# Kernel optimization log

Hardware: AMD Instinct MI355X
Metric: run time of the kernel (lower is better)

The kernel has to match this reference:

```python
import jax, jax.numpy as jnp
import numpy as np

N, C, DFF, TMAX = 4, 768, 3072, 20
RMS_EPS = 1e-6
SINK_EPS = 1e-6
POST_MULT = 2.0


def setup_inputs() -> dict:
    key = jax.random.key(0)
    ks = jax.random.split(key, 5)
    B, S = 4, 4096
    x = jax.random.normal(ks[0], (B, S, N, C), dtype=jnp.float32)
    phi = jax.random.normal(ks[1], (N * C, N * N + 2 * N), dtype=jnp.float32) * 0.02
    b = jnp.zeros((N * N + 2 * N,), dtype=jnp.float32)
    alpha_pre = jnp.ones((1,), dtype=jnp.float32)
    alpha_post = jnp.ones((1,), dtype=jnp.float32)
    alpha_res = jnp.ones((1,), dtype=jnp.float32)
    W1 = jax.random.normal(ks[2], (C, DFF), dtype=jnp.float32) * (1.0 / np.sqrt(C))
    b1 = jnp.zeros((DFF,), dtype=jnp.float32)
    W2 = jax.random.normal(ks[3], (DFF, C), dtype=jnp.float32) * (1.0 / np.sqrt(DFF))
    b2 = jnp.zeros((C,), dtype=jnp.float32)
    return {"x": x, "phi": phi, "b": b, "alpha_pre": alpha_pre,
            "alpha_post": alpha_post, "alpha_res": alpha_res,
            "W1": W1, "b1": b1, "W2": W2, "b2": b2}


def _sinkhorn(logits):
    # logits: (..., 16) -> doubly-stochastic (..., 4, 4); rows = logits[..., 4i:4i+4]
    r = logits.reshape(*logits.shape[:-1], N, N)
    r = jnp.exp(r - jnp.max(r, axis=-1, keepdims=True))
    for _ in range(TMAX):
        r = r / (jnp.sum(r, axis=-1, keepdims=True) + SINK_EPS)  # row normalize
        r = r / (jnp.sum(r, axis=-2, keepdims=True) + SINK_EPS)  # column normalize
    return r


def _mhc_forward(x, phi, b, alpha_pre, alpha_post, alpha_res, W1, b1, W2, b2):
    lead = x.shape[:-2]
    x_mat = x.reshape(-1, N * C)
    # fused RMS-norm + linear routing projection
    invr = jax.lax.rsqrt(jnp.mean(x_mat * x_mat, axis=-1, keepdims=True) + RMS_EPS)
    mix = (x_mat @ phi) * invr  # (T, n^2 + 2n)
    h_pre = jax.nn.sigmoid(mix[:, :N] * alpha_pre + b[:N]).reshape(*lead, N)
    h_post = (jax.nn.sigmoid(mix[:, N:2 * N] * alpha_post + b[N:2 * N]) * POST_MULT).reshape(*lead, N)
    h_res = _sinkhorn(mix[:, 2 * N:] * alpha_res + b[2 * N:]).reshape(*lead, N, N)
    # pre-aggregate n streams -> single full-width stream
    x_in = jnp.einsum('...nc,...n->...c', x, h_pre)
    # wrapped sublayer: baseline MLP at full width
    f_out = jax.nn.gelu(x_in @ W1 + b1, approximate=False) @ W2 + b2
    # residual stream mixing + post scatter
    res_gather = jnp.einsum('...ij,...jc->...ic', h_res, x)
    return res_gather + h_post[..., None] * f_out[..., None, :]


def reference(x, phi, b, alpha_pre, alpha_post, alpha_res, W1, b1, W2, b2):
    return _mhc_forward(x, phi, b, alpha_pre, alpha_post, alpha_res, W1, b1, W2, b2)
```

## Files before the change

### kernel.cpp

```cpp
#include <hip/hip_runtime.h>
#include <hip/hip_bf16.h>
#include <stdint.h>

#define NT   16384
#define C_   768
#define DFF_ 3072
#define KX   3072
#define NMIX 24

typedef __attribute__((ext_vector_type(8))) short shortx8;
typedef __attribute__((ext_vector_type(4))) float floatx4;

__device__ __forceinline__ short f2bf(float f) {
  union { float f; uint32_t u; } v; v.f = f;
  uint32_t r = v.u + 0x7fffu + ((v.u >> 16) & 1u);
  return (short)(r >> 16);
}

__global__ void phiT_kernel(const float* __restrict__ phi, float* __restrict__ phiT) {
  int idx = blockIdx.x * 256 + threadIdx.x;
  if (idx < KX * NMIX) {
    int k = idx / NMIX, j = idx - k * NMIX;
    phiT[(size_t)j * KX + k] = phi[idx];
  }
}

__global__ __launch_bounds__(256) void transpose_bf16(const float* __restrict__ in,
                                                      short* __restrict__ out,
                                                      int R, int C) {
  __shared__ float tile[32][33];
  int bx = blockIdx.x * 32;
  int by = blockIdx.y * 32;
  int tx = threadIdx.x & 31, ty = threadIdx.x >> 5;
  #pragma unroll
  for (int i = 0; i < 32; i += 8)
    tile[ty + i][tx] = in[(size_t)(by + ty + i) * C + bx + tx];
  __syncthreads();
  #pragma unroll
  for (int i = 0; i < 32; i += 8)
    out[(size_t)(bx + ty + i) * R + by + tx] = f2bf(tile[tx][ty + i]);
}

#define TB 64
__global__ __launch_bounds__(256) void k1(
    const float* __restrict__ x, const float* __restrict__ phiT,
    const float* __restrict__ bvec, const float* __restrict__ a_pre,
    const float* __restrict__ a_post, const float* __restrict__ a_res,
    short* __restrict__ x_in, float* __restrict__ hpost, float* __restrict__ hres) {
  __shared__ float xs[TB][132];
  __shared__ float invr_s[TB];
  __shared__ float mixs[TB][NMIX];
  __shared__ float hpre_s[TB][4];
  int tid = threadIdx.x;
  int lane = tid & 63;
  int w = tid >> 6;
  int wu = __builtin_amdgcn_readfirstlane(w);
  int t0 = blockIdx.x * TB;

  float acc[6] = {0.f, 0.f, 0.f, 0.f, 0.f, 0.f};
  float ssq = 0.f;

  for (int kc = 0; kc < KX; kc += 128) {
    if (kc) __syncthreads();
    #pragma unroll
    for (int jj = 0; jj < 8; ++jj) {
      int idx = tid + jj * 256;
      int row = idx >> 5, c4 = idx & 31;
      const float4 v = *(const float4*)&x[(size_t)(t0 + row) * KX + kc + c4 * 4];
      *(float4*)&xs[row][c4 * 4] = v;
    }
    __syncthreads();
    #pragma unroll 4
    for (int k4 = 0; k4 < 32; ++k4) {
      const float4 xv = *(const float4*)&xs[lane][k4 * 4];
      if (w == 0) ssq += xv.x * xv.x + xv.y * xv.y + xv.z * xv.z + xv.w * xv.w;
      int kk = kc + k4 * 4;
      #pragma unroll
      for (int jj = 0; jj < 6; ++jj) {
        const float4 p = *(const float4*)&phiT[(size_t)(wu * 6 + jj) * KX + kk];
        acc[jj] += p.x * xv.x + p.y * xv.y + p.z * xv.z + p.w * xv.w;
      }
    }
  }
  if (w == 0) invr_s[lane] = rsqrtf(ssq * (1.0f / KX) + 1e-6f);
  #pragma unroll
  for (int jj = 0; jj < 6; ++jj) mixs[lane][w * 6 + jj] = acc[jj];
  __syncthreads();

  {
    int tq = tid >> 2, r = tid & 3;
    float invr = invr_s[tq];
    float ares = a_res[0];
    float v0 = mixs[tq][8 + r * 4 + 0] * invr * ares + bvec[8 + r * 4 + 0];
    float v1 = mixs[tq][8 + r * 4 + 1] * invr * ares + bvec[8 + r * 4 + 1];
    float v2 = mixs[tq][8 + r * 4 + 2] * invr * ares + bvec[8 + r * 4 + 2];
    float v3 = mixs[tq][8 + r * 4 + 3] * invr * ares + bvec[8 + r * 4 + 3];
    float mx = fmaxf(fmaxf(v0, v1), fmaxf(v2, v3));
    v0 = __expf(v0 - mx); v1 = __expf(v1 - mx); v2 = __expf(v2 - mx); v3 = __expf(v3 - mx);
    for (int it = 0; it < 20; ++it) {
      float s = v0 + v1 + v2 + v3 + 1e-6f;
      float inv = 1.0f / s;
      v0 *= inv; v1 *= inv; v2 *= inv; v3 *= inv;
      float c0 = v0 + __shfl_xor(v0, 1); c0 += __shfl_xor(c0, 2);
      float c1 = v1 + __shfl_xor(v1, 1); c1 += __shfl_xor(c1, 2);
      float c2 = v2 + __shfl_xor(v2, 1); c2 += __shfl_xor(c2, 2);
      float c3 = v3 + __shfl_xor(v3, 1); c3 += __shfl_xor(c3, 2);
      v0 /= (c0 + 1e-6f); v1 /= (c1 + 1e-6f); v2 /= (c2 + 1e-6f); v3 /= (c3 + 1e-6f);
    }
    float* ho = hres + (size_t)(t0 + tq) * 16 + r * 4;
    ho[0] = v0; ho[1] = v1; ho[2] = v2; ho[3] = v3;
    if (r == 0) {
      float apre = a_pre[0];
      #pragma unroll
      for (int n = 0; n < 4; ++n) {
        float z = mixs[tq][n] * invr * apre + bvec[n];
        hpre_s[tq][n] = 1.0f / (1.0f + __expf(-z));
      }
    } else if (r == 1) {
      float apost = a_post[0];
      #pragma unroll
      for (int n = 0; n < 4; ++n) {
        float z = mixs[tq][4 + n] * invr * apost + bvec[4 + n];
        hpost[(size_t)(t0 + tq) * 4 + n] = 2.0f / (1.0f + __expf(-z));
      }
    }
  }
  __syncthreads();

  if (tid < 192) {
    int c = tid * 4;
    for (int t = 0; t < TB; ++t) {
      const float* xr = x + (size_t)(t0 + t) * KX + c;
      float4 x0 = *(const float4*)(xr);
      float4 x1 = *(const float4*)(xr + C_);
      float4 x2 = *(const float4*)(xr + 2 * C_);
      float4 x3 = *(const float4*)(xr + 3 * C_);
      float p0 = hpre_s[t][0], p1 = hpre_s[t][1], p2 = hpre_s[t][2], p3 = hpre_s[t][3];
      short4 s;
      s.x = f2bf(p0 * x0.x + p1 * x1.x + p2 * x2.x + p3 * x3.x);
      s.y = f2bf(p0 * x0.y + p1 * x1.y + p2 * x2.y + p3 * x3.y);
      s.z = f2bf(p0 * x0.z + p1 * x1.z + p2 * x2.z + p3 * x3.z);
      s.w = f2bf(p0 * x0.w + p1 * x1.w + p2 * x2.w + p3 * x3.w);
      *(short4*)&x_in[(size_t)(t0 + t) * C_ + c] = s;
    }
  }
}

template <int EPI>
__global__ __launch_bounds__(256, 3) void gemm_bt(
    const short* __restrict__ A, const short* __restrict__ B,
    int M, int N, int K, const float* __restrict__ bias,
    short* __restrict__ outb,
    const float* __restrict__ x, const float* __restrict__ hres,
    const float* __restrict__ hpost, float* __restrict__ out) {
  __shared__ short As[128 * 32];
  __shared__ short Bs[128 * 32];
  int tid = threadIdx.x;
  int lane = tid & 63, w = tid >> 6;
  int m0 = blockIdx.y * 128, n0 = blockIdx.x * 128;
  int wm = (w >> 1) * 64, wn = (w & 1) * 64;
  int lrow = lane & 15, quad = lane >> 4;
  floatx4 acc[4][4] = {};

  for (int k0 = 0; k0 < K; k0 += 32) {
    if (k0) __syncthreads();
    #pragma unroll
    for (int i = 0; i < 2; ++i) {
      int c = tid + i * 256;
      int row = c >> 2, slot = c & 3;
      const short* ga = A + (size_t)(m0 + row) * K + k0 + slot * 8;
      const short* gb = B + (size_t)(n0 + row) * K + k0 + slot * 8;
      __builtin_amdgcn_global_load_lds((const __attribute__((address_space(1))) void*)ga,
                                       (__attribute__((address_space(3))) void*)&As[c * 8],
                                       16, 0, 0);
      __builtin_amdgcn_global_load_lds((const __attribute__((address_space(1))) void*)gb,
                                       (__attribute__((address_space(3))) void*)&Bs[c * 8],
                                       16, 0, 0);
    }
    __syncthreads();
    shortx8 af[4], bfr[4];
    #pragma unroll
    for (int mi = 0; mi < 4; ++mi)
      af[mi] = *(const shortx8*)&As[(wm + mi * 16 + lrow) * 32 + quad * 8];
    #pragma unroll
    for (int ni = 0; ni < 4; ++ni)
      bfr[ni] = *(const shortx8*)&Bs[(wn + ni * 16 + lrow) * 32 + quad * 8];
    #pragma unroll
    for (int mi = 0; mi < 4; ++mi)
      #pragma unroll
      for (int ni = 0; ni < 4; ++ni)
        acc[mi][ni] = __builtin_amdgcn_mfma_f32_16x16x32_bf16(af[mi], bfr[ni], acc[mi][ni], 0, 0, 0);
  }

  float bcol[4];
  #pragma unroll
  for (int ni = 0; ni < 4; ++ni) bcol[ni] = bias[n0 + wn + ni * 16 + lrow];

  if (EPI == 1) {
    #pragma unroll
    for (int mi = 0; mi < 4; ++mi) {
      #pragma unroll
      for (int r = 0; r < 4; ++r) {
        int row = m0 + wm + mi * 16 + quad * 4 + r;
        #pragma unroll
        for (int ni = 0; ni < 4; ++ni) {
          int col = n0 + wn + ni * 16 + lrow;
          float v = acc[mi][ni][r] + bcol[ni];
          float g = 0.5f * v * (1.0f + erff(v * 0.70710678118654752f));
          outb[(size_t)row * N + col] = f2bf(g);
        }
      }
    }
  } else {
    #pragma unroll
    for (int mi = 0; mi < 4; ++mi) {
      #pragma unroll
      for (int r = 0; r < 4; ++r) {
        int row = m0 + wm + mi * 16 + quad * 4 + r;
        const float* hr = hres + (size_t)row * 16;
        const float* hp = hpost + (size_t)row * 4;
        const float* xr = x + (size_t)row * KX;
        float* orow = out + (size_t)row * KX;
        float hrv[16];
        #pragma unroll
        for (int q = 0; q < 16; ++q) hrv[q] = hr[q];
        float h0 = hp[0], h1 = hp[1], h2 = hp[2], h3 = hp[3];
        #pragma unroll
        for (int ni = 0; ni < 4; ++ni) {
          int col = n0 + wn + ni * 16 + lrow;
          float f = acc[mi][ni][r] + bcol[ni];
          float x0 = xr[col], x1 = xr[C_ + col], x2 = xr[2 * C_ + col], x3 = xr[3 * C_ + col];
          orow[col]            = hrv[0] * x0 + hrv[1] * x1 + hrv[2] * x2 + hrv[3] * x3 + h0 * f;
          orow[C_ + col]       = hrv[4] * x0 + hrv[5] * x1 + hrv[6] * x2 + hrv[7] * x3 + h1 * f;
          orow[2 * C_ + col]   = hrv[8] * x0 + hrv[9] * x1 + hrv[10] * x2 + hrv[11] * x3 + h2 * f;
          orow[3 * C_ + col]   = hrv[12] * x0 + hrv[13] * x1 + hrv[14] * x2 + hrv[15] * x3 + h3 * f;
        }
      }
    }
  }
}

extern "C" void kernel_launch(void* const* d_in, const int* in_sizes, int n_in,
                              void* d_out, int out_size, void* d_ws, size_t ws_size,
                              hipStream_t stream) {
  const float* x      = (const float*)d_in[0];
  const float* phi    = (const float*)d_in[1];
  const float* b      = (const float*)d_in[2];
  const float* a_pre  = (const float*)d_in[3];
  const float* a_post = (const float*)d_in[4];
  const float* a_res  = (const float*)d_in[5];
  const float* W1     = (const float*)d_in[6];
  const float* b1     = (const float*)d_in[7];
  const float* W2     = (const float*)d_in[8];
  const float* b2     = (const float*)d_in[9];
  float* out = (float*)d_out;

  char* ws = (char*)d_ws;
  size_t off = 0;
  auto carve = [&](size_t bytes) {
    char* p = ws + off;
    off += (bytes + 255) & ~(size_t)255;
    return p;
  };
  short* x_in  = (short*)carve((size_t)NT * C_ * 2);
  short* act   = (short*)carve((size_t)NT * DFF_ * 2);
  float* hpost = (float*)carve((size_t)NT * 4 * 4);
  float* hres  = (float*)carve((size_t)NT * 16 * 4);
  short* W1T   = (short*)carve((size_t)DFF_ * C_ * 2);
  short* W2T   = (short*)carve((size_t)C_ * DFF_ * 2);
  float* phiT  = (float*)carve((size_t)NMIX * KX * 4);

  phiT_kernel<<<dim3((KX * NMIX + 255) / 256), 256, 0, stream>>>(phi, phiT);
  transpose_bf16<<<dim3(DFF_ / 32, C_ / 32), 256, 0, stream>>>(W1, W1T, C_, DFF_);
  transpose_bf16<<<dim3(C_ / 32, DFF_ / 32), 256, 0, stream>>>(W2, W2T, DFF_, C_);
  k1<<<dim3(NT / TB), 256, 0, stream>>>(x, phiT, b, a_pre, a_post, a_res, x_in, hpost, hres);
  gemm_bt<1><<<dim3(DFF_ / 128, NT / 128), 256, 0, stream>>>(
      x_in, W1T, NT, DFF_, C_, b1, act, nullptr, nullptr, nullptr, nullptr);
  gemm_bt<2><<<dim3(C_ / 128, NT / 128), 256, 0, stream>>>(
      act, W2T, NT, C_, DFF_, b2, nullptr, x, hres, hpost, out);
}
```

Before: 820.2 us.

## Split routing projection over K into three kernels for more parallelism

The monolithic k1 kernel is split into three kernels. k1a computes partial projections and sum-of-squares over four K segments, which raises the block count from 256 to 1024. k1b reduces the partials and computes the sigmoid and Sinkhorn coefficients. k1c performs the pre-aggregation into bf16 with one fully parallel thread per four-column chunk, instead of the previous serial loop over 64 tokens run by 192 threads. This is meant to fix the low occupancy of the old kernel, which had only 256 blocks on a large GPU, at the cost of extra launches and partial-sum traffic through global memory.

```diff
diff --git a/kernel.cpp b/kernel.cpp
--- a/kernel.cpp
+++ b/kernel.cpp
@@ -7,6 +7,9 @@
 #define DFF_ 3072
 #define KX   3072
 #define NMIX 24
+#define TB   64
+#define KSPLIT 4
+#define KSEG (KX / KSPLIT)
 
 typedef __attribute__((ext_vector_type(8))) short shortx8;
 typedef __attribute__((ext_vector_type(4))) float floatx4;
@@ -41,27 +44,23 @@
     out[(size_t)(bx + ty + i) * R + by + tx] = f2bf(tile[tx][ty + i]);
 }
 
-#define TB 64
-__global__ __launch_bounds__(256) void k1(
+__global__ __launch_bounds__(256) void k1a(
     const float* __restrict__ x, const float* __restrict__ phiT,
-    const float* __restrict__ bvec, const float* __restrict__ a_pre,
-    const float* __restrict__ a_post, const float* __restrict__ a_res,
-    short* __restrict__ x_in, float* __restrict__ hpost, float* __restrict__ hres) {
+    float* __restrict__ pmix, float* __restrict__ pssq) {
   __shared__ float xs[TB][132];
-  __shared__ float invr_s[TB];
-  __shared__ float mixs[TB][NMIX];
-  __shared__ float hpre_s[TB][4];
   int tid = threadIdx.x;
   int lane = tid & 63;
   int w = tid >> 6;
   int wu = __builtin_amdgcn_readfirstlane(w);
-  int t0 = blockIdx.x * TB;
+  int t0 = (blockIdx.x >> 2) * TB;
+  int slot = blockIdx.x & 3;
+  int ks = slot * KSEG;
 
   float acc[6] = {0.f, 0.f, 0.f, 0.f, 0.f, 0.f};
   float ssq = 0.f;
 
-  for (int kc = 0; kc < KX; kc += 128) {
-    if (kc) __syncthreads();
+  for (int kc = ks; kc < ks + KSEG; kc += 128) {
+    if (kc != ks) __syncthreads();
     #pragma unroll
     for (int jj = 0; jj < 8; ++jj) {
       int idx = tid + jj * 256;
@@ -82,13 +81,42 @@
       }
     }
   }
-  if (w == 0) invr_s[lane] = rsqrtf(ssq * (1.0f / KX) + 1e-6f);
+  if (w == 0) pssq[(size_t)(t0 + lane) * KSPLIT + slot] = ssq;
   #pragma unroll
-  for (int jj = 0; jj < 6; ++jj) mixs[lane][w * 6 + jj] = acc[jj];
+  for (int jj = 0; jj < 6; ++jj)
+    pmix[((size_t)(t0 + lane) * KSPLIT + slot) * NMIX + wu * 6 + jj] = acc[jj];
+}
+
+__global__ __launch_bounds__(256) void k1b(
+    const float* __restrict__ pmix, const float* __restrict__ pssq,
+    const float* __restrict__ bvec, const float* __restrict__ a_pre,
+    const float* __restrict__ a_post, const float* __restrict__ a_res,
+    float* __restrict__ hpre, float* __restrict__ hpost, float* __restrict__ hres) {
+  __shared__ float mixs[TB][NMIX];
+  __shared__ float invr_s[TB];
+  int tid = threadIdx.x;
+  int t0 = blockIdx.x * TB;
+  int tq = tid >> 2, r = tid & 3;
+
+  {
+    const float* pm = pmix + (size_t)(t0 + tq) * KSPLIT * NMIX;
+    float s[6] = {0.f, 0.f, 0.f, 0.f, 0.f, 0.f};
+    #pragma unroll
+    for (int sl = 0; sl < KSPLIT; ++sl)
+      #pragma unroll
+      for (int jj = 0; jj < 6; ++jj)
+        s[jj] += pm[sl * NMIX + r * 6 + jj];
+    #pragma unroll
+    for (int jj = 0; jj < 6; ++jj) mixs[tq][r * 6 + jj] = s[jj];
+    if (r == 0) {
+      const float* ps = pssq + (size_t)(t0 + tq) * KSPLIT;
+      float sq = ps[0] + ps[1] + ps[2] + ps[3];
+      invr_s[tq] = rsqrtf(sq * (1.0f / KX) + 1e-6f);
+    }
+  }
   __syncthreads();
 
   {
-    int tq = tid >> 2, r = tid & 3;
     float invr = invr_s[tq];
     float ares = a_res[0];
     float v0 = mixs[tq][8 + r * 4 + 0] * invr * ares + bvec[8 + r * 4 + 0];
@@ -111,39 +139,42 @@
     ho[0] = v0; ho[1] = v1; ho[2] = v2; ho[3] = v3;
     if (r == 0) {
       float apre = a_pre[0];
-      #pragma unroll
-      for (int n = 0; n < 4; ++n) {
-        float z = mixs[tq][n] * invr * apre + bvec[n];
-        hpre_s[tq][n] = 1.0f / (1.0f + __expf(-z));
-      }
+      float4 hp;
+      hp.x = 1.0f / (1.0f + __expf(-(mixs[tq][0] * invr * apre + bvec[0])));
+      hp.y = 1.0f / (1.0f + __expf(-(mixs[tq][1] * invr * apre + bvec[1])));
+      hp.z = 1.0f / (1.0f + __expf(-(mixs[tq][2] * invr * apre + bvec[2])));
+      hp.w = 1.0f / (1.0f + __expf(-(mixs[tq][3] * invr * apre + bvec[3])));
+      *(float4*)&hpre[(size_t)(t0 + tq) * 4] = hp;
     } else if (r == 1) {
       float apost = a_post[0];
-      #pragma unroll
-      for (int n = 0; n < 4; ++n) {
-        float z = mixs[tq][4 + n] * invr * apost + bvec[4 + n];
-        hpost[(size_t)(t0 + tq) * 4 + n] = 2.0f / (1.0f + __expf(-z));
-      }
-    }
-  }
-  __syncthreads();
-
-  if (tid < 192) {
-    int c = tid * 4;
-    for (int t = 0; t < TB; ++t) {
-      const float* xr = x + (size_t)(t0 + t) * KX + c;
-      float4 x0 = *(const float4*)(xr);
-      float4 x1 = *(const float4*)(xr + C_);
-      float4 x2 = *(const float4*)(xr + 2 * C_);
-      float4 x3 = *(const float4*)(xr + 3 * C_);
-      float p0 = hpre_s[t][0], p1 = hpre_s[t][1], p2 = hpre_s[t][2], p3 = hpre_s[t][3];
-      short4 s;
-      s.x = f2bf(p0 * x0.x + p1 * x1.x + p2 * x2.x + p3 * x3.x);
-      s.y = f2bf(p0 * x0.y + p1 * x1.y + p2 * x2.y + p3 * x3.y);
-      s.z = f2bf(p0 * x0.z + p1 * x1.z + p2 * x2.z + p3 * x3.z);
-      s.w = f2bf(p0 * x0.w + p1 * x1.w + p2 * x2.w + p3 * x3.w);
-      *(short4*)&x_in[(size_t)(t0 + t) * C_ + c] = s;
-    }
-  }
+      float4 hq;
+      hq.x = 2.0f / (1.0f + __expf(-(mixs[tq][4] * invr * apost + bvec[4])));
+      hq.y = 2.0f / (1.0f + __expf(-(mixs[tq][5] * invr * apost + bvec[5])));
+      hq.z = 2.0f / (1.0f + __expf(-(mixs[tq][6] * invr * apost + bvec[6])));
+      hq.w = 2.0f / (1.0f + __expf(-(mixs[tq][7] * invr * apost + bvec[7])));
+      *(float4*)&hpost[(size_t)(t0 + tq) * 4] = hq;
+    }
+  }
+}
+
+__global__ __launch_bounds__(256) void k1c(
+    const float* __restrict__ x, const float* __restrict__ hpre,
+    short* __restrict__ x_in) {
+  int idx = blockIdx.x * 256 + threadIdx.x;
+  int t = idx / 192;
+  int c = (idx - t * 192) * 4;
+  float4 hp = *(const float4*)&hpre[(size_t)t * 4];
+  const float* xr = x + (size_t)t * KX + c;
+  float4 x0 = *(const float4*)(xr);
+  float4 x1 = *(const float4*)(xr + C_);
+  float4 x2 = *(const float4*)(xr + 2 * C_);
+  float4 x3 = *(const float4*)(xr + 3 * C_);
+  short4 s;
+  s.x = f2bf(hp.x * x0.x + hp.y * x1.x + hp.z * x2.x + hp.w * x3.x);
+  s.y = f2bf(hp.x * x0.y + hp.y * x1.y + hp.z * x2.y + hp.w * x3.y);
+  s.z = f2bf(hp.x * x0.z + hp.y * x1.z + hp.z * x2.z + hp.w * x3.z);
+  s.w = f2bf(hp.x * x0.w + hp.y * x1.w + hp.z * x2.w + hp.w * x3.w);
+  *(short4*)&x_in[(size_t)t * C_ + c] = s;
 }
 
 template <int EPI>
@@ -266,14 +297,20 @@
   short* act   = (short*)carve((size_t)NT * DFF_ * 2);
   float* hpost = (float*)carve((size_t)NT * 4 * 4);
   float* hres  = (float*)carve((size_t)NT * 16 * 4);
+  float* hpre  = (float*)carve((size_t)NT * 4 * 4);
   short* W1T   = (short*)carve((size_t)DFF_ * C_ * 2);
   short* W2T   = (short*)carve((size_t)C_ * DFF_ * 2);
   float* phiT  = (float*)carve((size_t)NMIX * KX * 4);
+  float* pmix  = (float*)carve((size_t)NT * KSPLIT * NMIX * 4);
+  float* pssq  = (float*)carve((size_t)NT * KSPLIT * 4);
 
   phiT_kernel<<<dim3((KX * NMIX + 255) / 256), 256, 0, stream>>>(phi, phiT);
   transpose_bf16<<<dim3(DFF_ / 32, C_ / 32), 256, 0, stream>>>(W1, W1T, C_, DFF_);
   transpose_bf16<<<dim3(C_ / 32, DFF_ / 32), 256, 0, stream>>>(W2, W2T, DFF_, C_);
-  k1<<<dim3(NT / TB), 256, 0, stream>>>(x, phiT, b, a_pre, a_post, a_res, x_in, hpost, hres);
+  k1a<<<dim3((NT / TB) * KSPLIT), 256, 0, stream>>>(x, phiT, pmix, pssq);
+  k1b<<<dim3(NT / TB), 256, 0, stream>>>(pmix, pssq, b, a_pre, a_post, a_res,
+                                         hpre, hpost, hres);
+  k1c<<<dim3(NT * 192 / 256), 256, 0, stream>>>(x, hpre, x_in);
   gemm_bt<1><<<dim3(DFF_ / 128, NT / 128), 256, 0, stream>>>(
       x_in, W1T, NT, DFF_, C_, b1, act, nullptr, nullptr, nullptr, nullptr);
   gemm_bt<2><<<dim3(C_ / 128, NT / 128), 256, 0, stream>>>(
```

New measurement: 717.3 us. -12.5%, faster.
